# Performance work log

Measured on AMD Instinct MI355X. Metric: run time of the kernel, lower is better.

## Reference

```python
import jax
jax.config.update("jax_enable_x64", True)
import jax.numpy as jnp
import numpy as np

CKA_WEIGHT = 0.1


def _group_cka_sum(feats):
    """feats: [F, N, D] float. Returns sum of pairwise CKA over all (i,j) pairs.

    Faithful to CKASR: K = X X^T with zeroed diagonal, unbiased HSIC
    (Song et al. estimator), CKA[i,j] = HSIC(Ki,Kj)/sqrt(HSIC(Ki,Ki)HSIC(Kj,Kj)).
    All pairwise loops are batched into einsums.
    """
    F, N, D = feats.shape
    X = feats.reshape(F, N, D).astype(jnp.float64)
    K = jnp.einsum('fnd,fmd->fnm', X, X)                 # [F,N,N] Gram
    K = K * (1.0 - jnp.eye(N, dtype=K.dtype))            # fill_diagonal_(0)
    # HSIC(Ki, Kj) = 1/(N(N-3)) * ( tr(Ki Kj)
    #   + sum(Ki) sum(Kj) / ((N-1)(N-2))
    #   - 2/(N-2) * <rowsum(Ki), rowsum(Kj)> )
    trKL = jnp.einsum('iab,jab->ij', K, K)               # tr(Ki Kj), K symmetric
    s = jnp.sum(K, axis=(1, 2))                          # [F] total sums
    r = jnp.sum(K, axis=2)                               # [F,N] row sums
    rr = jnp.einsum('ia,ja->ij', r, r)                   # [F,F]
    hsic = (trKL + jnp.outer(s, s) / ((N - 1) * (N - 2))
            - 2.0 * rr / (N - 2)) / (N * (N - 3))        # [F,F]
    d = jnp.sqrt(jnp.diagonal(hsic))                     # [F]
    cka = hsic / (d[:, None] * d[None, :])
    return jnp.sum(cka)


def setup_inputs() -> dict:
    key = jax.random.key(0)
    k1, k2, k3, k4 = jax.random.split(key, 4)
    N, C = 64, 1000
    output = jax.random.normal(k1, (N, C), dtype=jnp.float32)
    target = jax.random.randint(k2, (N,), 0, C, dtype=jnp.int64)
    feats_a = jax.random.normal(k3, (3, N, 65536), dtype=jnp.float32)
    feats_b = jax.random.normal(k4, (4, N, 32768), dtype=jnp.float32)
    return {"output": output, "target": target,
            "feats_a": feats_a, "feats_b": feats_b}


def reference(output, target, feats_a, feats_b):
    N = output.shape[0]
    logp = jax.nn.log_softmax(output.astype(jnp.float32), axis=-1)
    ce = -jnp.mean(logp[jnp.arange(N), target])           # CrossEntropyLoss (mean)
    cka = _group_cka_sum(feats_a) + _group_cka_sum(feats_b)
    loss = ce + CKA_WEIGHT * cka.astype(jnp.float32)
    return (loss, output)
```

## Files before the change

### kernel.cpp

```cpp
#include <hip/hip_runtime.h>
#include <math.h>

typedef __attribute__((ext_vector_type(8))) short short8;
typedef __attribute__((ext_vector_type(4))) float f32x4;
typedef __attribute__((ext_vector_type(16))) float f32x16;

#define PSTRIDE 4160

__device__ __forceinline__ unsigned int bf16_rn(float x) {
    unsigned int u = __float_as_uint(x);
    return (u + 0x7FFFu + ((u >> 16) & 1u)) >> 16;
}

__device__ __forceinline__ short8 cvt8(float4 a, float4 b) {
    short8 h;
    h[0] = (short)bf16_rn(a.x); h[1] = (short)bf16_rn(a.y);
    h[2] = (short)bf16_rn(a.z); h[3] = (short)bf16_rn(a.w);
    h[4] = (short)bf16_rn(b.x); h[5] = (short)bf16_rn(b.y);
    h[6] = (short)bf16_rn(b.z); h[7] = (short)bf16_rn(b.w);
    return h;
}

__global__ __launch_bounds__(512, 6) void gram_ce_kernel(
    const float* __restrict__ A, const float* __restrict__ B,
    float* __restrict__ partials, int nfA, int nfB,
    const float* __restrict__ logits, const int* __restrict__ target,
    float* __restrict__ out_copy, float* __restrict__ ce_rows, int ceCount)
{
    __shared__ float smem[4096];
    const int t = threadIdx.x;

    if ((int)blockIdx.x < ceCount) {
        const int row = blockIdx.x;
        const float* x = logits + row * 1000;
        float m = -INFINITY;
        for (int i = t; i < 1000; i += 512) {
            float v = x[i];
            out_copy[row * 1000 + i] = v;
            m = fmaxf(m, v);
        }
        smem[t] = m; __syncthreads();
        for (int s = 256; s > 0; s >>= 1) {
            if (t < s) smem[t] = fmaxf(smem[t], smem[t + s]);
            __syncthreads();
        }
        m = smem[0];
        __syncthreads();
        float ssum = 0.f;
        for (int i = t; i < 1000; i += 512) ssum += expf(x[i] - m);
        smem[t] = ssum; __syncthreads();
        for (int s = 256; s > 0; s >>= 1) {
            if (t < s) smem[t] += smem[t + s];
            __syncthreads();
        }
        if (t == 0) {
            double lse = (double)m + log((double)smem[0]);
            int tg = target[row];
            ce_rows[row] = (float)(-((double)x[tg] - lse));
        }
        return;
    }

    const int gb = blockIdx.x - ceCount;
    const int uA = nfA * 128;
    const float* xf;
    int c, D;
    if (gb < uA) {
        int f = gb >> 7; c = gb & 127; D = 65536;
        xf = A + (size_t)f * 64 * 65536;
    } else {
        int v = gb - uA;
        int f = v >> 6; c = v & 63; D = 32768;
        xf = B + (size_t)f * 64 * 32768;
    }

    const int wave = t >> 6, lane = t & 63;
    const int q = wave & 3, h = wave >> 2;
    const int wr = q >> 1, wc = q & 1;
    const int lr = lane & 31, hi = lane >> 5;
    const int k0 = c * 512 + h * 256 + hi * 8;

    const float* pA = xf + (size_t)(wr * 32 + lr) * D + k0;
    const float* pB = xf + (size_t)(wc * 32 + lr) * D + k0;

    f32x16 acc = (f32x16)0.f;
    if (wr == wc) {
#pragma unroll
        for (int s = 0; s < 16; ++s) {
            float4 a0 = *(const float4*)(pA + s * 16);
            float4 a1 = *(const float4*)(pA + s * 16 + 4);
            short8 fa = cvt8(a0, a1);
            acc = __builtin_amdgcn_mfma_f32_32x32x16_bf16(fa, fa, acc, 0, 0, 0);
        }
    } else {
#pragma unroll
        for (int s = 0; s < 16; ++s) {
            float4 a0 = *(const float4*)(pA + s * 16);
            float4 a1 = *(const float4*)(pA + s * 16 + 4);
            float4 b0 = *(const float4*)(pB + s * 16);
            float4 b1 = *(const float4*)(pB + s * 16 + 4);
            short8 fa = cvt8(a0, a1);
            short8 fb = cvt8(b0, b1);
            acc = __builtin_amdgcn_mfma_f32_32x32x16_bf16(fa, fb, acc, 0, 0, 0);
        }
    }

    float* qb = smem + q * 1024;
    if (h == 0) {
#pragma unroll
        for (int r = 0; r < 16; ++r) {
            int rl = (r & 3) + 8 * (r >> 2) + 4 * hi;
            qb[rl * 32 + lr] = acc[r];
        }
    }
    __syncthreads();
    if (h == 1) {
#pragma unroll
        for (int r = 0; r < 16; ++r) {
            int rl = (r & 3) + 8 * (r >> 2) + 4 * hi;
            qb[rl * 32 + lr] += acc[r];
        }
    }
    __syncthreads();

    float* outp = partials + (size_t)gb * PSTRIDE;
    const f32x4* s4 = (const f32x4*)smem;
    f32x4* o4 = (f32x4*)outp;
    for (int e = t; e < 1024; e += 512) {
        int qq = e >> 8, rl = (e >> 3) & 31, cl = e & 7;
        o4[((qq >> 1) * 32 + rl) * 16 + (qq & 1) * 8 + cl] = s4[e];
    }
}

__global__ __launch_bounds__(256) void reduce_kernel(
    const float* __restrict__ partials, float* __restrict__ K, int singleF)
{
    __shared__ double red[256];
    int f, eblk, base, count;
    if (singleF < 0) {
        f = blockIdx.x >> 6; eblk = blockIdx.x & 63;
        if (f < 3) { base = f * 128;            count = 128; }
        else       { base = 384 + (f - 3) * 64; count = 64;  }
    } else {
        f = singleF; eblk = blockIdx.x; base = 0;
        count = (f < 3) ? 128 : 64;
    }
    const int e = (eblk << 6) + (threadIdx.x & 63);
    const int jg = threadIdx.x >> 6;

    double s0 = 0.0, s1 = 0.0;
    for (int j = jg; j < count; j += 8) {
        s0 += (double)partials[(size_t)(base + j) * PSTRIDE + e];
        s1 += (double)partials[(size_t)(base + j + 4) * PSTRIDE + e];
    }
    red[threadIdx.x] = s0 + s1;
    __syncthreads();
    if (jg == 0) {
        double tot = red[threadIdx.x] + red[threadIdx.x + 64]
                   + red[threadIdx.x + 128] + red[threadIdx.x + 192];
        int rr = e >> 6, cc = e & 63;
        K[f * 4096 + e] = (rr == cc) ? 0.f : (float)tot;
    }
}

__global__ __launch_bounds__(256) void hsic_kernel(
    const float* __restrict__ K, double* __restrict__ hsic_out)
{
    const int p = blockIdx.x;
    int i, j;
    if (p < 9) { i = p / 3; j = p % 3; }
    else       { int q = p - 9; i = 3 + q / 4; j = 3 + q % 4; }
    const float* Ki = K + i * 4096;
    const float* Kj = K + j * 4096;
    const int t = threadIdx.x;

    __shared__ double red[256];
    __shared__ double ri[64], rj[64];

    double local = 0.0;
    for (int e = t; e < 4096; e += 256)
        local += (double)Ki[e] * (double)Kj[e];
    red[t] = local; __syncthreads();
    for (int s = 128; s > 0; s >>= 1) {
        if (t < s) red[t] += red[t + s];
        __syncthreads();
    }

    if (t < 64) {
        double s = 0.0;
        for (int mc = 0; mc < 64; ++mc) s += (double)Ki[t * 64 + mc];
        ri[t] = s;
    } else if (t < 128) {
        int n = t - 64;
        double s = 0.0;
        for (int mc = 0; mc < 64; ++mc) s += (double)Kj[n * 64 + mc];
        rj[n] = s;
    }
    __syncthreads();

    if (t == 0) {
        double tr = red[0];
        double rr = 0.0, si = 0.0, sj = 0.0;
        for (int n = 0; n < 64; ++n) {
            rr += ri[n] * rj[n];
            si += ri[n];
            sj += rj[n];
        }
        const double N = 64.0;
        const double c1 = (N - 1.0) * (N - 2.0);
        const double c2 = N - 2.0;
        const double c3 = N * (N - 3.0);
        hsic_out[p] = (tr + si * sj / c1 - 2.0 * rr / c2) / c3;
    }
}

__global__ __launch_bounds__(64) void final_kernel(
    const double* __restrict__ hsic, const float* __restrict__ ce_rows,
    float* __restrict__ out_loss)
{
    if (threadIdx.x != 0) return;
    double ce = 0.0;
    for (int n = 0; n < 64; ++n) ce += (double)ce_rows[n];
    ce /= 64.0;

    double cka_total = 0.0;
    for (int i = 0; i < 3; ++i)
        for (int j = 0; j < 3; ++j)
            cka_total += hsic[i * 3 + j] / sqrt(hsic[i * 3 + i] * hsic[j * 3 + j]);
    for (int i = 0; i < 4; ++i)
        for (int j = 0; j < 4; ++j)
            cka_total += hsic[9 + i * 4 + j] / sqrt(hsic[9 + i * 4 + i] * hsic[9 + j * 4 + j]);

    out_loss[0] = (float)(ce + 0.1 * cka_total);
}

extern "C" void kernel_launch(void* const* d_in, const int* in_sizes, int n_in,
                              void* d_out, int out_size, void* d_ws, size_t ws_size,
                              hipStream_t stream)
{
    const float* output  = (const float*)d_in[0];
    const int*   target  = (const int*)d_in[1];
    const float* feats_a = (const float*)d_in[2];
    const float* feats_b = (const float*)d_in[3];
    float* out = (float*)d_out;

    char* ws = (char*)d_ws;
    float*  K        = (float*)ws;
    float*  ce_rows  = (float*)(ws + 114688);
    double* hsic     = (double*)(ws + 114944);
    float*  partials = (float*)(ws + 131072);

    const size_t partMain = (size_t)640 * PSTRIDE * 4;
    const size_t mainNeed = 131072 + partMain;

    if (ws_size >= mainNeed) {
        hipLaunchKernelGGL(gram_ce_kernel, dim3(640 + 64), dim3(512), 0, stream,
                           feats_a, feats_b, partials, 3, 4,
                           output, target, out + 1, ce_rows, 64);
        hipLaunchKernelGGL(reduce_kernel, dim3(448), dim3(256), 0, stream,
                           partials, K, -1);
    } else {
        for (int f = 0; f < 7; ++f) {
            if (f < 3) {
                const float* X = feats_a + (size_t)f * 64 * 65536;
                int ce = (f == 0) ? 64 : 0;
                hipLaunchKernelGGL(gram_ce_kernel, dim3(128 + ce), dim3(512), 0, stream,
                                   X, (const float*)nullptr, partials, 1, 0,
                                   output, target, out + 1, ce_rows, ce);
            } else {
                const float* X = feats_b + (size_t)(f - 3) * 64 * 32768;
                hipLaunchKernelGGL(gram_ce_kernel, dim3(64), dim3(512), 0, stream,
                                   (const float*)nullptr, X, partials, 0, 1,
                                   output, target, out + 1, ce_rows, 0);
            }
            hipLaunchKernelGGL(reduce_kernel, dim3(64), dim3(256), 0, stream,
                               partials, K, f);
        }
    }

    hipLaunchKernelGGL(hsic_kernel, dim3(25), dim3(256), 0, stream, K, hsic);
    hipLaunchKernelGGL(final_kernel, dim3(1), dim3(64), 0, stream,
                       hsic, ce_rows, out);
}
```

Before: 157.6 us.

## Exploit Gram symmetry: skip duplicate off-diagonal tile, rebalance waves across K

The 64x64 Gram tile was computed as four 32x32 quadrants, so the two off-diagonal quadrants did the same work twice. Each block now computes one off-diagonal quadrant, split over four waves, and the two diagonal quadrants, each split over two waves. The missing quadrant is filled in by transposing from shared memory at write-out. Partial results are now combined with LDS atomicAdd, the output loop writes scalar floats instead of float4, and the launch-bounds occupancy hint goes from 6 to 8.

```diff
diff --git a/kernel.cpp b/kernel.cpp
--- a/kernel.cpp
+++ b/kernel.cpp
@@ -21,7 +21,7 @@
     return h;
 }
 
-__global__ __launch_bounds__(512, 6) void gram_ce_kernel(
+__global__ __launch_bounds__(512, 8) void gram_ce_kernel(
     const float* __restrict__ A, const float* __restrict__ B,
     float* __restrict__ partials, int nfA, int nfB,
     const float* __restrict__ logits, const int* __restrict__ target,
@@ -75,26 +75,15 @@
     }
 
     const int wave = t >> 6, lane = t & 63;
-    const int q = wave & 3, h = wave >> 2;
-    const int wr = q >> 1, wc = q & 1;
     const int lr = lane & 31, hi = lane >> 5;
-    const int k0 = c * 512 + h * 256 + hi * 8;
-
-    const float* pA = xf + (size_t)(wr * 32 + lr) * D + k0;
-    const float* pB = xf + (size_t)(wc * 32 + lr) * D + k0;
 
     f32x16 acc = (f32x16)0.f;
-    if (wr == wc) {
-#pragma unroll
-        for (int s = 0; s < 16; ++s) {
-            float4 a0 = *(const float4*)(pA + s * 16);
-            float4 a1 = *(const float4*)(pA + s * 16 + 4);
-            short8 fa = cvt8(a0, a1);
-            acc = __builtin_amdgcn_mfma_f32_32x32x16_bf16(fa, fa, acc, 0, 0, 0);
-        }
-    } else {
-#pragma unroll
-        for (int s = 0; s < 16; ++s) {
+    if (wave < 4) {
+        const int k0 = c * 512 + wave * 128 + hi * 8;
+        const float* pA = xf + (size_t)lr * D + k0;
+        const float* pB = xf + (size_t)(32 + lr) * D + k0;
+#pragma unroll
+        for (int s = 0; s < 8; ++s) {
             float4 a0 = *(const float4*)(pA + s * 16);
             float4 a1 = *(const float4*)(pA + s * 16 + 4);
             float4 b0 = *(const float4*)(pB + s * 16);
@@ -103,32 +92,50 @@
             short8 fb = cvt8(b0, b1);
             acc = __builtin_amdgcn_mfma_f32_32x32x16_bf16(fa, fb, acc, 0, 0, 0);
         }
-    }
-
-    float* qb = smem + q * 1024;
-    if (h == 0) {
+    } else {
+        const int rb = (wave >= 6) ? 32 : 0;
+        const int k0 = c * 512 + (wave & 1) * 256 + hi * 8;
+        const float* pA = xf + (size_t)(rb + lr) * D + k0;
+#pragma unroll
+        for (int s = 0; s < 16; ++s) {
+            float4 a0 = *(const float4*)(pA + s * 16);
+            float4 a1 = *(const float4*)(pA + s * 16 + 4);
+            short8 fa = cvt8(a0, a1);
+            acc = __builtin_amdgcn_mfma_f32_32x32x16_bf16(fa, fa, acc, 0, 0, 0);
+        }
+    }
+
+    float* buf = (wave < 4) ? (smem + 2048)
+               : ((wave < 6) ? smem : (smem + 1024));
+    const bool writer = (wave == 0) || (wave == 4) || (wave == 6);
+    if (writer) {
 #pragma unroll
         for (int r = 0; r < 16; ++r) {
             int rl = (r & 3) + 8 * (r >> 2) + 4 * hi;
-            qb[rl * 32 + lr] = acc[r];
-        }
-    }
-    __syncthreads();
-    if (h == 1) {
+            buf[rl * 32 + lr] = acc[r];
+        }
+    }
+    __syncthreads();
+    if (!writer) {
 #pragma unroll
         for (int r = 0; r < 16; ++r) {
             int rl = (r & 3) + 8 * (r >> 2) + 4 * hi;
-            qb[rl * 32 + lr] += acc[r];
+            atomicAdd(&buf[rl * 32 + lr], acc[r]);
         }
     }
     __syncthreads();
 
     float* outp = partials + (size_t)gb * PSTRIDE;
-    const f32x4* s4 = (const f32x4*)smem;
-    f32x4* o4 = (f32x4*)outp;
-    for (int e = t; e < 1024; e += 512) {
-        int qq = e >> 8, rl = (e >> 3) & 31, cl = e & 7;
-        o4[((qq >> 1) * 32 + rl) * 16 + (qq & 1) * 8 + cl] = s4[e];
+    for (int e = t; e < 4096; e += 512) {
+        int rr = e >> 6, cc = e & 63;
+        float v;
+        if (rr < 32)
+            v = (cc < 32) ? smem[rr * 32 + cc]
+                          : smem[2048 + rr * 32 + (cc - 32)];
+        else
+            v = (cc < 32) ? smem[2048 + cc * 32 + (rr - 32)]
+                          : smem[1024 + (rr - 32) * 32 + (cc - 32)];
+        outp[e] = v;
     }
 }
 
```

After: 160.3 us. Within noise of the previous version (+1.7%).
